# Kernel optimization log

Measured on AMD Instinct MI355X. Metric: run time of the kernel, lower is better.

## Reference

```python
import jax, jax.numpy as jnp
import numpy as np

SIGMA = 1.0
NDCG_AT_K = 10
EPS = 1e-8


def setup_inputs() -> dict:
    key = jax.random.key(0)
    k1, k2 = jax.random.split(key)
    B, N = 64, 1024
    scores = jax.random.normal(k1, (B, N), dtype=jnp.float32)
    relevances = jax.random.randint(k2, (B, N), 0, 2, dtype=jnp.int32)
    return {"scores": scores, "relevances": relevances}


def reference(scores, relevances):
    # scores: [B, N] float, relevances: [B, N] binary int
    B, N = scores.shape
    y = relevances.astype(jnp.float32)
    rel = y > 0          # [B, N] relevant items (i indices)
    nonrel = y == 0      # [B, N] non-relevant items (j indices)

    pos = jnp.arange(N, dtype=jnp.float32)
    disc = 1.0 / jnp.log2(pos + 2.0)  # DCG discount per position index

    # Ideal DCG@k: sort relevances descending, discounted sum of top-k
    y_sorted = -jnp.sort(-y, axis=-1)
    idcg = jnp.sum(y_sorted[:, :NDCG_AT_K] * disc[:NDCG_AT_K], axis=-1)  # [B]

    # Batches with no rel, no non-rel, or zero idcg are skipped (contribute 0 pairs)
    valid_b = rel.any(axis=-1) & nonrel.any(axis=-1) & (idcg > 0)

    pair_mask = rel[:, :, None] & nonrel[:, None, :] & valid_b[:, None, None]  # [B,N,N]

    # |Delta NDCG| for swapping positions i and j (binary gains 1 vs 0)
    delta = jnp.abs(disc[None, :] - disc[:, None])[None, :, :] / (idcg[:, None, None] + EPS)

    s_diff = scores[:, :, None] - scores[:, None, :]  # [B, N, N]
    pair_loss = delta * jax.nn.softplus(-SIGMA * s_diff)

    total = jnp.sum(jnp.where(pair_mask, pair_loss, 0.0))
    num_pairs = jnp.sum(pair_mask)
    # reduction == 'mean': global mean over all pairs across the batch
    loss = jnp.where(num_pairs > 0, total / num_pairs.astype(jnp.float32), 0.0)
    return loss
```

## Files before the change

### kernel.cpp

```cpp
#include <hip/hip_runtime.h>


#define NPOS   1024
#define SPLIT  16
#define KTOP   10
#define EPSF   1e-8f
#define MAXSL  ((NPOS + SPLIT - 1) / SPLIT)
#define MAXB   64
#define LOG2E  1.4426950408889634f
#define LN2    0.6931471805599453

__device__ const float IDCG_S[11] = {
    0.0f, 1.0f, 1.63092975f, 2.13092975f, 2.56160631f, 2.94845912f,
    3.30466631f, 3.63799964f, 3.95346452f, 4.25449452f, 4.54355935f
};

__device__ __forceinline__ float softplus_log2(float zp) {
    const float t = __builtin_amdgcn_exp2f(-fabsf(zp));
    const float g = t * (1.442216f + t * (-0.701718f
                  + t * (0.365639f + t * (-0.106478f))));
    return fmaxf(zp, 0.0f) + g;
}

__device__ __forceinline__ float inv_log2_f(float x) {
    return __builtin_amdgcn_rcpf(__log2f(x));
}

__global__ __launch_bounds__(256) void lr_pair_kernel(
    const float* __restrict__ scores,
    const int*   __restrict__ relev,
    double*      __restrict__ partials,
    unsigned*    __restrict__ pairCnt)
{
    __shared__ __align__(16) float2 nshr[NPOS];
    __shared__ float2 rshr[MAXSL];
    __shared__ int    cnt[16];
    __shared__ double wsum[4];

    const int b     = blockIdx.x >> 4;
    const int slice = blockIdx.x & (SPLIT - 1);
    const int tid   = threadIdx.x;
    const int lane  = tid & 63;
    const int wave  = tid >> 6;

    const float* srow = scores + (size_t)b * NPOS;
    const int*   rrow = relev  + (size_t)b * NPOS;

    float sv[4], dv[4]; int rposv[4]; bool rf[4];
    #pragma unroll
    for (int it = 0; it < 4; ++it) {
        const int c = it * 4 + wave, idx = c * 64 + lane;
        sv[it] = srow[idx] * LOG2E;
        dv[it] = inv_log2_f((float)idx + 2.0f);
        const bool r = rrow[idx] > 0; rf[it] = r;
        unsigned long long m = __ballot(r);
        rposv[it] = __popcll(m & ((1ull << lane) - 1ull));
        if (lane == 0) cnt[c] = __popcll(m);
    }
    __syncthreads();

    int nrel = 0;
    #pragma unroll
    for (int c = 0; c < 16; ++c) nrel += cnt[c];
    const int nnon = NPOS - nrel;
    const int i0 = (slice * nrel) / SPLIT;
    const int i1 = ((slice + 1) * nrel) / SPLIT;
    const int ni = i1 - i0;

    {
        int rb = 0;
        for (int cc = 0; cc < wave; ++cc) rb += cnt[cc];
        #pragma unroll
        for (int it = 0; it < 4; ++it) {
            const int c = it * 4 + wave;
            if (rf[it]) {
                const int p = rb + rposv[it];
                if (p >= i0 && p < i1) rshr[p - i0] = make_float2(sv[it], dv[it]);
            } else {
                nshr[c * 64 - rb + (lane - rposv[it])] = make_float2(sv[it], dv[it]);
            }
            if (it < 3) rb += cnt[c] + cnt[c+1] + cnt[c+2] + cnt[c+3];
        }
    }

    const float idcg = IDCG_S[min(nrel, KTOP)];
    __syncthreads();

    double block_total = 0.0;
    if (nrel > 0 && nnon > 0 && ni > 0) {
        const float4* nshr4 = reinterpret_cast<const float4*>(nshr);
        const int nnon2 = nnon >> 1;

        float acc0 = 0.f, acc1 = 0.f, acc2 = 0.f, acc3 = 0.f;
        int i = 0;
        for (; i + 4 <= ni; i += 4) {
            const float2 a0 = rshr[i], a1 = rshr[i+1], a2 = rshr[i+2], a3 = rshr[i+3];
            for (int jj = tid; jj < nnon2; jj += 256) {
                const float4 q = nshr4[jj];
                acc0 += fabsf(a0.y - q.y) * softplus_log2(q.x - a0.x);
                acc1 += fabsf(a1.y - q.y) * softplus_log2(q.x - a1.x);
                acc2 += fabsf(a2.y - q.y) * softplus_log2(q.x - a2.x);
                acc3 += fabsf(a3.y - q.y) * softplus_log2(q.x - a3.x);
                acc0 += fabsf(a0.y - q.w) * softplus_log2(q.z - a0.x);
                acc1 += fabsf(a1.y - q.w) * softplus_log2(q.z - a1.x);
                acc2 += fabsf(a2.y - q.w) * softplus_log2(q.z - a2.x);
                acc3 += fabsf(a3.y - q.w) * softplus_log2(q.z - a3.x);
            }
        }
        for (; i < ni; ++i) {
            const float2 a0 = rshr[i];
            for (int jj = tid; jj < nnon2; jj += 256) {
                const float4 q = nshr4[jj];
                acc0 += fabsf(a0.y - q.y) * softplus_log2(q.x - a0.x);
                acc1 += fabsf(a0.y - q.w) * softplus_log2(q.z - a0.x);
            }
        }
        if (nnon & 1) {
            const float2 bj = nshr[nnon - 1];
            if (tid < ni) {
                const float2 a = rshr[tid];
                acc0 += fabsf(a.y - bj.y) * softplus_log2(bj.x - a.x);
            }
        }
        float acc = (acc0 + acc1) + (acc2 + acc3);

        #pragma unroll
        for (int off = 32; off >= 1; off >>= 1) acc += __shfl_down(acc, off);
        if (lane == 0) wsum[wave] = (double)acc;
        __syncthreads();
        if (tid == 0)
            block_total = (wsum[0] + wsum[1] + wsum[2] + wsum[3])
                        * ((double)(1.0f / (idcg + EPSF)) * LN2);
    }

    if (tid == 0) {
        partials[blockIdx.x] = block_total;
        if (slice == 0)
            pairCnt[b] = (nrel > 0 && nnon > 0) ? (unsigned)(nrel * nnon) : 0u;
    }
}

__global__ __launch_bounds__(256) void lr_final_kernel(
    const double*   __restrict__ partials,
    const unsigned* __restrict__ pairCnt,
    float*          __restrict__ out,
    int B, int nparts)
{
    __shared__ double    dsh[4];
    __shared__ long long psh[4];

    const int tid = threadIdx.x, lane = tid & 63, wave = tid >> 6;

    double tot = 0.0;
    for (int k = tid; k < nparts; k += 256) tot += partials[k];
    long long pairs = (tid < B) ? (long long)pairCnt[tid] : 0;

    #pragma unroll
    for (int off = 32; off >= 1; off >>= 1) {
        tot   += __shfl_down(tot, off);
        pairs += __shfl_down(pairs, off);
    }
    if (lane == 0) { dsh[wave] = tot; psh[wave] = pairs; }
    __syncthreads();
    if (tid == 0) {
        double    tt = dsh[0] + dsh[1] + dsh[2] + dsh[3];
        long long np = psh[0] + psh[1] + psh[2] + psh[3];
        out[0] = (np > 0) ? (float)(tt / (double)np) : 0.0f;
    }
}

extern "C" void kernel_launch(void* const* d_in, const int* in_sizes, int n_in,
                              void* d_out, int out_size, void* d_ws, size_t ws_size,
                              hipStream_t stream) {
    const float* scores = (const float*)d_in[0];
    const int*   relev  = (const int*)d_in[1];
    float*       out    = (float*)d_out;
    const int    B      = in_sizes[0] / NPOS;
    const int    nparts = B * SPLIT;

    double*   partials = (double*)d_ws;
    unsigned* pairCnt  = (unsigned*)(partials + nparts);

    lr_pair_kernel<<<nparts, 256, 0, stream>>>(scores, relev, partials, pairCnt);
    lr_final_kernel<<<1, 256, 0, stream>>>(partials, pairCnt, out, B, nparts);
}
```

Before: 66.67 us.

## Fuse final reduction into pair kernel via fixed-point atomic last-block completion

Removes the separate finalization kernel and the double-precision partials array. Each block atomically adds a fixed-point encoded partial with a packed arrival counter into a per-batch accumulator. The last block per batch forwards to a global accumulator, and the last batch writes the mean. Accumulators are initialised by a device-to-device copy from the relevance input, whose values are subtracted back as baselines, trading a kernel launch for a small memcpy and reduced fixed-point precision.

New measurement: 68.48 us. 1.03x slower.

```diff
diff --git a/kernel.cpp b/kernel.cpp
--- a/kernel.cpp
+++ b/kernel.cpp
@@ -9,6 +9,9 @@
 #define MAXB   64
 #define LOG2E  1.4426950408889634f
 #define LN2    0.6931471805599453
+#define FPSCALE 268435456.0
+#define BCNT_SHIFT 53
+#define GCNT_SHIFT 57
 
 __device__ const float IDCG_S[11] = {
     0.0f, 1.0f, 1.63092975f, 2.13092975f, 2.56160631f, 2.94845912f,
@@ -29,8 +32,10 @@
 __global__ __launch_bounds__(256) void lr_pair_kernel(
     const float* __restrict__ scores,
     const int*   __restrict__ relev,
-    double*      __restrict__ partials,
-    unsigned*    __restrict__ pairCnt)
+    unsigned long long* __restrict__ batch_acc,
+    unsigned long long* __restrict__ global_acc,
+    unsigned*           __restrict__ pairs_acc,
+    float*              __restrict__ out)
 {
     __shared__ __align__(16) float2 nshr[NPOS];
     __shared__ float2 rshr[MAXSL];
@@ -134,38 +139,35 @@
     }
 
     if (tid == 0) {
-        partials[blockIdx.x] = block_total;
-        if (slice == 0)
-            pairCnt[b] = (nrel > 0 && nnon > 0) ? (unsigned)(nrel * nnon) : 0u;
-    }
-}
-
-__global__ __launch_bounds__(256) void lr_final_kernel(
-    const double*   __restrict__ partials,
-    const unsigned* __restrict__ pairCnt,
-    float*          __restrict__ out,
-    int B, int nparts)
-{
-    __shared__ double    dsh[4];
-    __shared__ long long psh[4];
-
-    const int tid = threadIdx.x, lane = tid & 63, wave = tid >> 6;
-
-    double tot = 0.0;
-    for (int k = tid; k < nparts; k += 256) tot += partials[k];
-    long long pairs = (tid < B) ? (long long)pairCnt[tid] : 0;
-
-    #pragma unroll
-    for (int off = 32; off >= 1; off >>= 1) {
-        tot   += __shfl_down(tot, off);
-        pairs += __shfl_down(pairs, off);
-    }
-    if (lane == 0) { dsh[wave] = tot; psh[wave] = pairs; }
-    __syncthreads();
-    if (tid == 0) {
-        double    tt = dsh[0] + dsh[1] + dsh[2] + dsh[3];
-        long long np = psh[0] + psh[1] + psh[2] + psh[3];
-        out[0] = (np > 0) ? (float)(tt / (double)np) : 0.0f;
+        const unsigned long long fp =
+            (unsigned long long)(block_total * FPSCALE + 0.5);
+        const unsigned long long Kb =
+            (unsigned long long)(unsigned)relev[2 * b]
+          | ((unsigned long long)(unsigned)relev[2 * b + 1] << 32);
+        const unsigned long long old =
+            atomicAdd(&batch_acc[b], (1ull << BCNT_SHIFT) | fp);
+        const unsigned long long seen = old - Kb;
+        if ((seen >> BCNT_SHIFT) == SPLIT - 1) {
+            const unsigned long long bfp =
+                (seen & ((1ull << BCNT_SHIFT) - 1)) + fp;
+            if (nrel > 0 && nnon > 0)
+                atomicAdd(pairs_acc, (unsigned)(nrel * nnon));
+            const unsigned long long Kg =
+                (unsigned long long)(unsigned)relev[128]
+              | ((unsigned long long)(unsigned)relev[129] << 32);
+            const unsigned long long g = __hip_atomic_fetch_add(
+                global_acc, (1ull << GCNT_SHIFT) | bfp,
+                __ATOMIC_ACQ_REL, __HIP_MEMORY_SCOPE_AGENT);
+            const unsigned long long gseen = g - Kg;
+            if ((gseen >> GCNT_SHIFT) == MAXB - 1) {
+                const unsigned Kp = (unsigned)relev[130];
+                const unsigned np = atomicAdd(pairs_acc, 0u) - Kp;
+                const double tot =
+                    (double)((gseen & ((1ull << GCNT_SHIFT) - 1)) + bfp)
+                    * (1.0 / FPSCALE);
+                out[0] = (np > 0) ? (float)(tot / (double)np) : 0.0f;
+            }
+        }
     }
 }
 
@@ -178,9 +180,15 @@
     const int    B      = in_sizes[0] / NPOS;
     const int    nparts = B * SPLIT;
 
-    double*   partials = (double*)d_ws;
-    unsigned* pairCnt  = (unsigned*)(partials + nparts);
+    unsigned long long* batch_acc  = (unsigned long long*)d_ws;
+    unsigned long long* global_acc = batch_acc + MAXB;
+    unsigned*           pairs_acc  = (unsigned*)(global_acc + 1);
 
-    lr_pair_kernel<<<nparts, 256, 0, stream>>>(scores, relev, partials, pairCnt);
-    lr_final_kernel<<<1, 256, 0, stream>>>(partials, pairCnt, out, B, nparts);
+    hipMemcpyAsync(d_ws, d_in[1],
+                   (MAXB + 1) * sizeof(unsigned long long) + sizeof(unsigned),
+                   hipMemcpyDeviceToDevice, stream);
+
+    lr_pair_kernel<<<nparts, 256, 0, stream>>>(scores, relev,
+                                               batch_acc, global_acc,
+                                               pairs_acc, out);
 }
```
